# Optimization experiments

Measured on AMD Instinct MI355X. Metric: run time of the kernel, lower is better.

Reference implementation:

```python
import jax, jax.numpy as jnp
import numpy as np

D_MODEL = 1024
N_HEADS = 16
HEAD_DIM = 64
BATCH = 4
SEQ = 2048


def setup_inputs() -> dict:
    key = jax.random.key(0)
    ks = jax.random.split(key, 5)
    scale = 1.0 / np.sqrt(D_MODEL)
    return {
        "x": jax.random.normal(ks[0], (BATCH, SEQ, D_MODEL), dtype=jnp.float32),
        "Wq": jax.random.normal(ks[1], (D_MODEL, N_HEADS * HEAD_DIM), dtype=jnp.float32) * scale,
        "Wk": jax.random.normal(ks[2], (D_MODEL, N_HEADS * HEAD_DIM), dtype=jnp.float32) * scale,
        "Wv": jax.random.normal(ks[3], (D_MODEL, N_HEADS * HEAD_DIM), dtype=jnp.float32) * scale,
        "Wo": jax.random.normal(ks[4], (N_HEADS * HEAD_DIM, D_MODEL), dtype=jnp.float32) * scale,
        "bo": jnp.zeros((D_MODEL,), dtype=jnp.float32),
    }


def reference(x, Wq, Wk, Wv, Wo, bo):
    B, S, _ = x.shape
    H, Dh = N_HEADS, HEAD_DIM
    # projections -> [B, H, S, Dh]
    q = (x @ Wq).reshape(B, S, H, Dh).transpose(0, 2, 1, 3)
    k = (x @ Wk).reshape(B, S, H, Dh).transpose(0, 2, 1, 3)
    v = (x @ Wv).reshape(B, S, H, Dh).transpose(0, 2, 1, 3)
    score = jnp.einsum("bhsd,bhtd->bhst", q, k) / jnp.sqrt(jnp.float32(Dh))
    causal = jnp.triu(jnp.ones((S, S), dtype=bool), k=1)
    score = jnp.where(causal, -jnp.inf, score)
    attn_probs = jax.nn.softmax(score, axis=-1)
    # dropout is identity in eval mode
    attn = jnp.einsum("bhst,bhtd->bhsd", attn_probs, v)
    out = attn.transpose(0, 2, 1, 3).reshape(B, S, H * Dh)
    out = out @ Wo + bo
    return (out, attn_probs)
```

## Files before the change

kernel.cpp:

```cpp
#include <hip/hip_runtime.h>
#include <hip/hip_bf16.h>

typedef __attribute__((ext_vector_type(8))) short bf16x8;
typedef __attribute__((ext_vector_type(4))) float f32x4;
typedef unsigned short ushort_t;
typedef unsigned int uint_t;

#define AS1 __attribute__((address_space(1)))
#define AS3 __attribute__((address_space(3)))

__device__ __forceinline__ void gload_lds16(const void* g, void* l) {
    __builtin_amdgcn_global_load_lds((const AS1 void*)g, (AS3 void*)l, 16, 0, 0);
}

__device__ __forceinline__ ushort_t f2b(float f) {
    unsigned u = __builtin_bit_cast(unsigned, f);
    unsigned r = (u + 0x7FFFu + ((u >> 16) & 1u)) >> 16;
    return (ushort_t)r;
}

__global__ __launch_bounds__(256) void convert_x_kernel(const float* __restrict__ in,
                                                        ushort_t* __restrict__ out, int n4) {
    int i = blockIdx.x * blockDim.x + threadIdx.x;
    if (i < n4) {
        float4 f = ((const float4*)in)[i];
        ushort4 u;
        u.x = f2b(f.x); u.y = f2b(f.y); u.z = f2b(f.z); u.w = f2b(f.w);
        ((ushort4*)out)[i] = u;
    }
}

__global__ __launch_bounds__(256) void transpose_w_kernel(const float* __restrict__ W,
                                                          ushort_t* __restrict__ WT) {
    __shared__ float t[32][33];
    int n0 = blockIdx.x * 32, k0 = blockIdx.y * 32;
    int tx = threadIdx.x, ty = threadIdx.y;
    for (int i = 0; i < 4; ++i)
        t[ty + i * 8][tx] = W[(size_t)(k0 + ty + i * 8) * 1024 + n0 + tx];
    __syncthreads();
    for (int i = 0; i < 4; ++i)
        WT[(size_t)(n0 + ty + i * 8) * 1024 + k0 + tx] = f2b(t[tx][ty + i * 8]);
}

template <int N, int OUT_BF16>
__global__ __launch_bounds__(256) void gemm_kernel(const ushort_t* __restrict__ A,
                                                   const ushort_t* __restrict__ BT,
                                                   ushort_t* __restrict__ Cb,
                                                   float* __restrict__ Cf,
                                                   const float* __restrict__ bias) {
    const int K = 1024;
    __shared__ ushort_t As[2 * 128 * 32];
    __shared__ ushort_t Bs[2 * 128 * 32];
    int tid = threadIdx.x;
    int wid = tid >> 6, lane = tid & 63;
    int g = lane >> 4, lr = lane & 15;
    int m0 = blockIdx.x * 128, n0 = blockIdx.y * 128;
    int wm = wid >> 1, wn = wid & 1;

    f32x4 acc[4][4] = {};

    int c0 = wid * 2;
    int lrow = lane >> 2;
    int lcol = ((lane & 3) ^ ((lane >> 3) & 3)) * 8;
    const ushort_t* Ag0 = A  + (size_t)(m0 + c0 * 16 + lrow) * K + lcol;
    const ushort_t* Ag1 = A  + (size_t)(m0 + c0 * 16 + 16 + lrow) * K + lcol;
    const ushort_t* Bg0 = BT + (size_t)(n0 + c0 * 16 + lrow) * K + lcol;
    const ushort_t* Bg1 = BT + (size_t)(n0 + c0 * 16 + 16 + lrow) * K + lcol;

    int swzA = ((lr >> 1) & 3) << 4;

    auto stage = [&](int bufi, int kt) {
        char* a0 = (char*)As + bufi * 8192 + c0 * 1024;
        char* b0 = (char*)Bs + bufi * 8192 + c0 * 1024;
        gload_lds16(Ag0 + kt * 32, a0);
        gload_lds16(Ag1 + kt * 32, a0 + 1024);
        gload_lds16(Bg0 + kt * 32, b0);
        gload_lds16(Bg1 + kt * 32, b0 + 1024);
    };

    stage(0, 0);
    __syncthreads();
    int buf = 0;
    for (int kt = 0; kt < K / 32; ++kt) {
        if (kt + 1 < K / 32) stage(buf ^ 1, kt + 1);
        const char* ab = (const char*)As + buf * 8192;
        const char* bb = (const char*)Bs + buf * 8192;
        bf16x8 af[4], bfr[4];
#pragma unroll
        for (int m = 0; m < 4; ++m) {
            int row = wm * 64 + m * 16 + lr;
            af[m] = *(const bf16x8*)(ab + row * 64 + ((g * 16) ^ swzA));
        }
#pragma unroll
        for (int n = 0; n < 4; ++n) {
            int row = wn * 64 + n * 16 + lr;
            bfr[n] = *(const bf16x8*)(bb + row * 64 + ((g * 16) ^ swzA));
        }
#pragma unroll
        for (int m = 0; m < 4; ++m)
#pragma unroll
            for (int n = 0; n < 4; ++n)
                acc[m][n] = __builtin_amdgcn_mfma_f32_16x16x32_bf16(af[m], bfr[n], acc[m][n], 0, 0, 0);
        __syncthreads();
        buf ^= 1;
    }

#pragma unroll
    for (int m = 0; m < 4; ++m)
#pragma unroll
        for (int n = 0; n < 4; ++n) {
            int row0 = m0 + wm * 64 + m * 16 + g * 4;
            int col  = n0 + wn * 64 + n * 16 + lr;
#pragma unroll
            for (int r = 0; r < 4; ++r) {
                float v = acc[m][n][r];
                if (OUT_BF16)
                    Cb[(size_t)(row0 + r) * N + col] = f2b(v);
                else
                    Cf[(size_t)(row0 + r) * N + col] = v + bias[col];
            }
        }
}

__global__ __launch_bounds__(256) void vt_kernel(const ushort_t* __restrict__ Cqkv,
                                                 ushort_t* __restrict__ Vt) {
    int b = blockIdx.z, h = blockIdx.y, st = blockIdx.x;
    __shared__ ushort_t t[64][72];
    const ushort_t* src = Cqkv + (size_t)b * 2048 * 3072 + 2048 + (size_t)h * 64;
    int tid = threadIdx.x;
#pragma unroll
    for (int i = 0; i < 2; ++i) {
        int c = tid + i * 256;
        int sl = c >> 3, dc = (c & 7) * 8;
        *(bf16x8*)&t[sl][dc] = *(const bf16x8*)(src + (size_t)(st * 64 + sl) * 3072 + dc);
    }
    __syncthreads();
#pragma unroll
    for (int i = 0; i < 2; ++i) {
        int c = tid + i * 256;
        int d = c >> 3, sc = (c & 7) * 8;
        bf16x8 v;
#pragma unroll
        for (int j = 0; j < 8; ++j) v[j] = (short)t[sc + j][d];
        *(bf16x8*)(Vt + ((size_t)(b * 16 + h) * 64 + d) * 2048 + st * 64 + sc) = v;
    }
}

__global__ __launch_bounds__(256) void attn_kernel(const ushort_t* __restrict__ Cqkv,
                                                   const ushort_t* __restrict__ Vtg,
                                                   float* __restrict__ Pout,
                                                   ushort_t* __restrict__ Oout) {
    const int S = 2048, DQ = 3072;
    const float C1 = 0.18033688f;
    const float C2 = 5.77078016f;

    int z = (int)blockIdx.x + 32 * (int)blockIdx.y + 512 * (int)blockIdx.z;
    int h = (z >> 5) & 15, b = z >> 9;
    int qt = ((z & 31) + 13 * ((z >> 8) & 7)) & 31;
    int q0 = qt * 64;

    int tid = threadIdx.x, wid = tid >> 6, lane = tid & 63;
    int g = lane >> 4, lr = lane & 15;

    __shared__ ushort_t Ks[2][4096];
    __shared__ ushort_t Vs[2][4096];
    __shared__ ushort_t Pl[4096];
    char* PlB = (char*)Pl + wid * 2048;

    const ushort_t* Qb = Cqkv + (size_t)b * S * DQ + (size_t)h * 64;
    const ushort_t* Kb = Cqkv + (size_t)b * S * DQ + 1024 + (size_t)h * 64;
    const ushort_t* Vb = Vtg + (size_t)((b * 16 + h) * 64) * 2048;
    float* Pbase = Pout + (((size_t)(b * 16 + h)) * S + q0) * S;

    int srow = lane >> 3;
    int scol = ((lane & 7) ^ srow) * 8;

    auto stageK = [&](int bufi, int tt) {
        char* dst = (char*)&Ks[bufi][0] + wid * 1024;
        gload_lds16(Kb + (size_t)(tt * 64 + wid * 8 + srow) * DQ + scol, dst);
        gload_lds16(Kb + (size_t)(tt * 64 + 32 + wid * 8 + srow) * DQ + scol, dst + 4096);
    };
    auto stageV = [&](int bufi, int tt) {
        char* dst = (char*)&Vs[bufi][0] + wid * 1024;
        gload_lds16(Vb + (size_t)(wid * 8 + srow) * 2048 + tt * 64 + scol, dst);
        gload_lds16(Vb + (size_t)(32 + wid * 8 + srow) * 2048 + tt * 64 + scol, dst + 4096);
    };

    bf16x8 qf[2];
    {
        const ushort_t* qp = Qb + (size_t)(q0 + wid * 16 + lr) * DQ + g * 8;
        qf[0] = *(const bf16x8*)qp;
        qf[1] = *(const bf16x8*)(qp + 32);
    }
    int qloc = wid * 16 + lr;

    float psum = 0.f;
    stageK(0, 0);
    __syncthreads();
    int buf = 0;
    for (int tt = 0; tt <= qt; ++tt) {
        if (tt < qt) stageK(buf ^ 1, tt + 1);
        const char* ksb = (const char*)&Ks[buf][0];
#pragma unroll
        for (int nb = 0; nb < 4; ++nb) {
            int row = nb * 16 + lr;
            int x = (row & 7) << 4;
            f32x4 s = {};
            s = __builtin_amdgcn_mfma_f32_16x16x32_bf16(*(const bf16x8*)(ksb + row * 128 + ((g * 16) ^ x)), qf[0], s, 0, 0, 0);
            s = __builtin_amdgcn_mfma_f32_16x16x32_bf16(*(const bf16x8*)(ksb + row * 128 + ((64 + g * 16) ^ x)), qf[1], s, 0, 0, 0);
            if (tt == qt) {
#pragma unroll
                for (int r = 0; r < 4; ++r)
                    if (nb * 16 + g * 4 + r <= qloc) psum += exp2f(fmaf(s[r], C1, -C2));
            } else {
#pragma unroll
                for (int r = 0; r < 4; ++r) psum += exp2f(fmaf(s[r], C1, -C2));
            }
        }
        __syncthreads();
        buf ^= 1;
    }
    psum += __shfl_xor(psum, 16);
    psum += __shfl_xor(psum, 32);
    float lnl2 = __log2f(psum) + C2;

    f32x4 Oacc[4] = {};
    stageK(buf, 0);
    stageV(buf, 0);
    __syncthreads();
    for (int tt = 0; tt <= qt; ++tt) {
        if (tt < qt) { stageK(buf ^ 1, tt + 1); stageV(buf ^ 1, tt + 1); }
        const char* ksb = (const char*)&Ks[buf][0];
        const char* vsb = (const char*)&Vs[buf][0];
        f32x4 p[4];
#pragma unroll
        for (int nb = 0; nb < 4; ++nb) {
            int row = nb * 16 + lr;
            int x = (row & 7) << 4;
            f32x4 s = {};
            s = __builtin_amdgcn_mfma_f32_16x16x32_bf16(*(const bf16x8*)(ksb + row * 128 + ((g * 16) ^ x)), qf[0], s, 0, 0, 0);
            s = __builtin_amdgcn_mfma_f32_16x16x32_bf16(*(const bf16x8*)(ksb + row * 128 + ((64 + g * 16) ^ x)), qf[1], s, 0, 0, 0);
#pragma unroll
            for (int r = 0; r < 4; ++r) {
                float v = exp2f(fmaf(s[r], C1, -lnl2));
                if (tt == qt && (nb * 16 + g * 4 + r > qloc)) v = 0.f;
                p[nb][r] = v;
            }
        }
#pragma unroll
        for (int nb = 0; nb < 4; ++nb)
            *(f32x4*)(Pbase + (size_t)qloc * S + tt * 64 + nb * 16 + g * 4) = p[nb];
#pragma unroll
        for (int nb = 0; nb < 4; ++nb) {
            uint_t w0, w1;
            asm("v_cvt_pk_bf16_f32 %0, %1, %2" : "=v"(w0) : "v"(p[nb][0]), "v"(p[nb][1]));
            asm("v_cvt_pk_bf16_f32 %0, %1, %2" : "=v"(w1) : "v"(p[nb][2]), "v"(p[nb][3]));
            uint2 w; w.x = w0; w.y = w1;
            *(uint2*)(PlB + ((lr * 128 + nb * 32 + g * 8) ^ ((lr & 7) << 4))) = w;
        }
        __builtin_amdgcn_wave_barrier();
#pragma unroll
        for (int kc = 0; kc < 2; ++kc) {
            bf16x8 pf = *(const bf16x8*)(PlB + ((lr * 128 + kc * 64 + g * 16) ^ ((lr & 7) << 4)));
#pragma unroll
            for (int nb = 0; nb < 4; ++nb) {
                int vrow = nb * 16 + lr;
                bf16x8 vf = *(const bf16x8*)(vsb + vrow * 128 + ((kc * 64 + g * 16) ^ ((vrow & 7) << 4)));
                Oacc[nb] = __builtin_amdgcn_mfma_f32_16x16x32_bf16(pf, vf, Oacc[nb], 0, 0, 0);
            }
        }
        asm volatile("s_waitcnt vmcnt(4)" ::: "memory");
        __builtin_amdgcn_s_barrier();
        __builtin_amdgcn_sched_barrier(0);
        buf ^= 1;
    }

    {
        int vsr = tid >> 2, vsc = (tid & 3) * 16;
        float4 zf = {0.f, 0.f, 0.f, 0.f};
        for (int tt = qt + 1; tt < 32; ++tt) {
            float* dst = Pbase + (size_t)vsr * S + tt * 64 + vsc;
#pragma unroll
            for (int j = 0; j < 4; ++j) ((float4*)dst)[j] = zf;
        }
    }

#pragma unroll
    for (int nb = 0; nb < 4; ++nb)
#pragma unroll
        for (int r = 0; r < 4; ++r) {
            int q = q0 + wid * 16 + g * 4 + r;
            Oout[((size_t)b * S + q) * 1024 + h * 64 + nb * 16 + lr] = f2b(Oacc[nb][r]);
        }
}

extern "C" void kernel_launch(void* const* d_in, const int* in_sizes, int n_in,
                              void* d_out, int out_size, void* d_ws, size_t ws_size,
                              hipStream_t stream) {
    const float* x  = (const float*)d_in[0];
    const float* Wq = (const float*)d_in[1];
    const float* Wk = (const float*)d_in[2];
    const float* Wv = (const float*)d_in[3];
    const float* Wo = (const float*)d_in[4];
    const float* bo = (const float*)d_in[5];

    float* out  = (float*)d_out;
    float* Pout = out + (size_t)8388608;

    char* ws = (char*)d_ws;
    ushort_t* xb    = (ushort_t*)(ws);
    ushort_t* wqkv  = (ushort_t*)(ws + (16u << 20));
    ushort_t* wob   = (ushort_t*)(ws + (22u << 20));
    ushort_t* Cqkv  = (ushort_t*)(ws + (24u << 20));
    ushort_t* Vtw   = (ushort_t*)(ws + (72u << 20));
    ushort_t* attnb = (ushort_t*)(ws + (104u << 20));

    convert_x_kernel<<<8192, 256, 0, stream>>>(x, xb, 2097152);
    transpose_w_kernel<<<dim3(32, 32), dim3(32, 8), 0, stream>>>(Wq, wqkv);
    transpose_w_kernel<<<dim3(32, 32), dim3(32, 8), 0, stream>>>(Wk, wqkv + 1024 * 1024);
    transpose_w_kernel<<<dim3(32, 32), dim3(32, 8), 0, stream>>>(Wv, wqkv + 2 * 1024 * 1024);
    transpose_w_kernel<<<dim3(32, 32), dim3(32, 8), 0, stream>>>(Wo, wob);

    gemm_kernel<3072, 1><<<dim3(64, 24), 256, 0, stream>>>(xb, wqkv, Cqkv, nullptr, nullptr);

    vt_kernel<<<dim3(32, 16, 4), 256, 0, stream>>>(Cqkv, Vtw);

    attn_kernel<<<dim3(32, 16, 4), 256, 0, stream>>>(Cqkv, Vtw, Pout, attnb);

    gemm_kernel<1024, 0><<<dim3(64, 8), 256, 0, stream>>>(attnb, wob, nullptr, out, bo);
}
```

Before: 485.8 us.

## Fuse V transpose into QKV GEMM, remap GEMM blocks, deepen K prefetch, set wave priority

The QKV GEMM now writes the V columns straight into the transposed Vt layout, which removes the separate vt_kernel launch and its extra round trip through memory. Both GEMMs remap workgroup IDs in an XCD-aware order, aiming for better L2 locality. The first attention pass now keeps three K tiles in flight through a four-slot ring with vmcnt-based waits, and s_setprio is raised around the MFMA sections. The Vt stores from the GEMM are 8-byte strided writes, which may be less efficient than the old transpose kernel's writes.

```diff
diff --git a/kernel.cpp b/kernel.cpp
--- a/kernel.cpp
+++ b/kernel.cpp
@@ -42,19 +42,25 @@
         WT[(size_t)(n0 + ty + i * 8) * 1024 + k0 + tx] = f2b(t[tx][ty + i * 8]);
 }
 
-template <int N, int OUT_BF16>
+template <int N, int MODE>
 __global__ __launch_bounds__(256) void gemm_kernel(const ushort_t* __restrict__ A,
                                                    const ushort_t* __restrict__ BT,
                                                    ushort_t* __restrict__ Cb,
                                                    float* __restrict__ Cf,
-                                                   const float* __restrict__ bias) {
+                                                   const float* __restrict__ bias,
+                                                   ushort_t* __restrict__ Vt) {
     const int K = 1024;
     __shared__ ushort_t As[2 * 128 * 32];
     __shared__ ushort_t Bs[2 * 128 * 32];
     int tid = threadIdx.x;
     int wid = tid >> 6, lane = tid & 63;
     int g = lane >> 4, lr = lane & 15;
-    int m0 = blockIdx.x * 128, n0 = blockIdx.y * 128;
+
+    int z = (int)blockIdx.x + 64 * (int)blockIdx.y;
+    int nwg = 64 * (int)gridDim.y;
+    int zs = (z & 7) * (nwg >> 3) + (z >> 3);
+    int m0 = (zs % 64) * 128, n0 = (zs / 64) * 128;
+
     int wm = wid >> 1, wn = wid & 1;
 
     f32x4 acc[4][4] = {};
@@ -105,44 +111,35 @@
         buf ^= 1;
     }
 
-#pragma unroll
-    for (int m = 0; m < 4; ++m)
-#pragma unroll
-        for (int n = 0; n < 4; ++n) {
-            int row0 = m0 + wm * 64 + m * 16 + g * 4;
-            int col  = n0 + wn * 64 + n * 16 + lr;
-#pragma unroll
-            for (int r = 0; r < 4; ++r) {
-                float v = acc[m][n][r];
-                if (OUT_BF16)
-                    Cb[(size_t)(row0 + r) * N + col] = f2b(v);
-                else
-                    Cf[(size_t)(row0 + r) * N + col] = v + bias[col];
-            }
-        }
-}
-
-__global__ __launch_bounds__(256) void vt_kernel(const ushort_t* __restrict__ Cqkv,
-                                                 ushort_t* __restrict__ Vt) {
-    int b = blockIdx.z, h = blockIdx.y, st = blockIdx.x;
-    __shared__ ushort_t t[64][72];
-    const ushort_t* src = Cqkv + (size_t)b * 2048 * 3072 + 2048 + (size_t)h * 64;
-    int tid = threadIdx.x;
-#pragma unroll
-    for (int i = 0; i < 2; ++i) {
-        int c = tid + i * 256;
-        int sl = c >> 3, dc = (c & 7) * 8;
-        *(bf16x8*)&t[sl][dc] = *(const bf16x8*)(src + (size_t)(st * 64 + sl) * 3072 + dc);
-    }
-    __syncthreads();
-#pragma unroll
-    for (int i = 0; i < 2; ++i) {
-        int c = tid + i * 256;
-        int d = c >> 3, sc = (c & 7) * 8;
-        bf16x8 v;
-#pragma unroll
-        for (int j = 0; j < 8; ++j) v[j] = (short)t[sc + j][d];
-        *(bf16x8*)(Vt + ((size_t)(b * 16 + h) * 64 + d) * 2048 + st * 64 + sc) = v;
+    if (MODE == 2 && (n0 + wn * 64) >= 2048) {
+#pragma unroll
+        for (int m = 0; m < 4; ++m)
+#pragma unroll
+            for (int n = 0; n < 4; ++n) {
+                int row0 = m0 + wm * 64 + m * 16 + g * 4;
+                int c    = n0 + wn * 64 + n * 16 + lr - 2048;
+                int bb2 = row0 >> 11, sloc = row0 & 2047;
+                ushort4 u;
+                u.x = f2b(acc[m][n][0]); u.y = f2b(acc[m][n][1]);
+                u.z = f2b(acc[m][n][2]); u.w = f2b(acc[m][n][3]);
+                *(ushort4*)(Vt + ((size_t)(bb2 * 1024 + c)) * 2048 + sloc) = u;
+            }
+    } else {
+#pragma unroll
+        for (int m = 0; m < 4; ++m)
+#pragma unroll
+            for (int n = 0; n < 4; ++n) {
+                int row0 = m0 + wm * 64 + m * 16 + g * 4;
+                int col  = n0 + wn * 64 + n * 16 + lr;
+#pragma unroll
+                for (int r = 0; r < 4; ++r) {
+                    float v = acc[m][n][r];
+                    if (MODE == 0)
+                        Cf[(size_t)(row0 + r) * N + col] = v + bias[col];
+                    else
+                        Cb[(size_t)(row0 + r) * N + col] = f2b(v);
+                }
+            }
     }
 }
 
@@ -162,8 +159,7 @@
     int tid = threadIdx.x, wid = tid >> 6, lane = tid & 63;
     int g = lane >> 4, lr = lane & 15;
 
-    __shared__ ushort_t Ks[2][4096];
-    __shared__ ushort_t Vs[2][4096];
+    __shared__ ushort_t KV[4][4096];
     __shared__ ushort_t Pl[4096];
     char* PlB = (char*)Pl + wid * 2048;
 
@@ -175,13 +171,13 @@
     int srow = lane >> 3;
     int scol = ((lane & 7) ^ srow) * 8;
 
-    auto stageK = [&](int bufi, int tt) {
-        char* dst = (char*)&Ks[bufi][0] + wid * 1024;
+    auto stageK = [&](int ri, int tt) {
+        char* dst = (char*)&KV[ri][0] + wid * 1024;
         gload_lds16(Kb + (size_t)(tt * 64 + wid * 8 + srow) * DQ + scol, dst);
         gload_lds16(Kb + (size_t)(tt * 64 + 32 + wid * 8 + srow) * DQ + scol, dst + 4096);
     };
-    auto stageV = [&](int bufi, int tt) {
-        char* dst = (char*)&Vs[bufi][0] + wid * 1024;
+    auto stageV = [&](int ri, int tt) {
+        char* dst = (char*)&KV[2 + ri][0] + wid * 1024;
         gload_lds16(Vb + (size_t)(wid * 8 + srow) * 2048 + tt * 64 + scol, dst);
         gload_lds16(Vb + (size_t)(32 + wid * 8 + srow) * 2048 + tt * 64 + scol, dst + 4096);
     };
@@ -196,11 +192,15 @@
 
     float psum = 0.f;
     stageK(0, 0);
-    __syncthreads();
-    int buf = 0;
+    stageK(1, qt >= 1 ? 1 : 0);
+    asm volatile("s_waitcnt vmcnt(8)" ::: "memory");
+    __builtin_amdgcn_s_barrier();
+    __builtin_amdgcn_sched_barrier(0);
     for (int tt = 0; tt <= qt; ++tt) {
-        if (tt < qt) stageK(buf ^ 1, tt + 1);
-        const char* ksb = (const char*)&Ks[buf][0];
+        int nt = tt + 2;
+        stageK(nt & 3, nt <= qt ? nt : qt);
+        const char* ksb = (const char*)&KV[tt & 3][0];
+        __builtin_amdgcn_s_setprio(1);
 #pragma unroll
         for (int nb = 0; nb < 4; ++nb) {
             int row = nb * 16 + lr;
@@ -217,22 +217,26 @@
                 for (int r = 0; r < 4; ++r) psum += exp2f(fmaf(s[r], C1, -C2));
             }
         }
-        __syncthreads();
-        buf ^= 1;
+        __builtin_amdgcn_s_setprio(0);
+        asm volatile("s_waitcnt vmcnt(8)" ::: "memory");
+        __builtin_amdgcn_s_barrier();
+        __builtin_amdgcn_sched_barrier(0);
     }
     psum += __shfl_xor(psum, 16);
     psum += __shfl_xor(psum, 32);
     float lnl2 = __log2f(psum) + C2;
 
     f32x4 Oacc[4] = {};
-    stageK(buf, 0);
-    stageV(buf, 0);
+    stageK(0, 0);
+    stageV(0, 0);
     __syncthreads();
+    int buf = 0;
     for (int tt = 0; tt <= qt; ++tt) {
         if (tt < qt) { stageK(buf ^ 1, tt + 1); stageV(buf ^ 1, tt + 1); }
-        const char* ksb = (const char*)&Ks[buf][0];
-        const char* vsb = (const char*)&Vs[buf][0];
+        const char* ksb = (const char*)&KV[buf][0];
+        const char* vsb = (const char*)&KV[2 + buf][0];
         f32x4 p[4];
+        __builtin_amdgcn_s_setprio(1);
 #pragma unroll
         for (int nb = 0; nb < 4; ++nb) {
             int row = nb * 16 + lr;
@@ -247,6 +251,7 @@
                 p[nb][r] = v;
             }
         }
+        __builtin_amdgcn_s_setprio(0);
 #pragma unroll
         for (int nb = 0; nb < 4; ++nb)
             *(f32x4*)(Pbase + (size_t)qloc * S + tt * 64 + nb * 16 + g * 4) = p[nb];
@@ -259,6 +264,7 @@
             *(uint2*)(PlB + ((lr * 128 + nb * 32 + g * 8) ^ ((lr & 7) << 4))) = w;
         }
         __builtin_amdgcn_wave_barrier();
+        __builtin_amdgcn_s_setprio(1);
 #pragma unroll
         for (int kc = 0; kc < 2; ++kc) {
             bf16x8 pf = *(const bf16x8*)(PlB + ((lr * 128 + kc * 64 + g * 16) ^ ((lr & 7) << 4)));
@@ -269,6 +275,7 @@
                 Oacc[nb] = __builtin_amdgcn_mfma_f32_16x16x32_bf16(pf, vf, Oacc[nb], 0, 0, 0);
             }
         }
+        __builtin_amdgcn_s_setprio(0);
         asm volatile("s_waitcnt vmcnt(4)" ::: "memory");
         __builtin_amdgcn_s_barrier();
         __builtin_amdgcn_sched_barrier(0);
@@ -321,11 +328,9 @@
     transpose_w_kernel<<<dim3(32, 32), dim3(32, 8), 0, stream>>>(Wv, wqkv + 2 * 1024 * 1024);
     transpose_w_kernel<<<dim3(32, 32), dim3(32, 8), 0, stream>>>(Wo, wob);
 
-    gemm_kernel<3072, 1><<<dim3(64, 24), 256, 0, stream>>>(xb, wqkv, Cqkv, nullptr, nullptr);
-
-    vt_kernel<<<dim3(32, 16, 4), 256, 0, stream>>>(Cqkv, Vtw);
+    gemm_kernel<3072, 2><<<dim3(64, 24), 256, 0, stream>>>(xb, wqkv, Cqkv, nullptr, nullptr, Vtw);
 
     attn_kernel<<<dim3(32, 16, 4), 256, 0, stream>>>(Cqkv, Vtw, Pout, attnb);
 
-    gemm_kernel<1024, 0><<<dim3(64, 8), 256, 0, stream>>>(attnb, wob, nullptr, out, bo);
-}
+    gemm_kernel<1024, 0><<<dim3(64, 8), 256, 0, stream>>>(attnb, wob, nullptr, out, bo, nullptr);
+}
```

Measured after the change: 508.8 us. +4.7%, slower.

## Restructure attention for occupancy, triple-buffer GEMM, remap GEMM blocks, merge weight transposes

Applied to the files above, without the earlier changes.

Several changes at once. The attention kernel shrinks LDS to single-buffered K/V with a smaller P scratch and adds launch bounds for higher occupancy. It also interleaves the zero-fill of masked probability tiles into the main loops and uses s_setprio around MFMA sections. The GEMM moves to a three-stage LDS pipeline with explicit vmcnt waits and a remapped block order for cache locality. The four weight transposes merge into one launch. The cost is that attention loses its K/V prefetch overlap in the second pass.

```diff
diff --git a/kernel.cpp b/kernel.cpp
--- a/kernel.cpp
+++ b/kernel.cpp
@@ -30,9 +30,16 @@
     }
 }
 
-__global__ __launch_bounds__(256) void transpose_w_kernel(const float* __restrict__ W,
-                                                          ushort_t* __restrict__ WT) {
+__global__ __launch_bounds__(256) void transpose_w4_kernel(const float* __restrict__ W0,
+                                                           const float* __restrict__ W1,
+                                                           const float* __restrict__ W2,
+                                                           const float* __restrict__ W3,
+                                                           ushort_t* __restrict__ WTqkv,
+                                                           ushort_t* __restrict__ WTo) {
     __shared__ float t[32][33];
+    int which = blockIdx.z;
+    const float* W = (which == 0) ? W0 : (which == 1) ? W1 : (which == 2) ? W2 : W3;
+    ushort_t* WT = (which < 3) ? (WTqkv + (size_t)which * 1024 * 1024) : WTo;
     int n0 = blockIdx.x * 32, k0 = blockIdx.y * 32;
     int tx = threadIdx.x, ty = threadIdx.y;
     for (int i = 0; i < 4; ++i)
@@ -49,12 +56,17 @@
                                                    float* __restrict__ Cf,
                                                    const float* __restrict__ bias) {
     const int K = 1024;
-    __shared__ ushort_t As[2 * 128 * 32];
-    __shared__ ushort_t Bs[2 * 128 * 32];
+    __shared__ ushort_t As[3 * 128 * 32];
+    __shared__ ushort_t Bs[3 * 128 * 32];
     int tid = threadIdx.x;
     int wid = tid >> 6, lane = tid & 63;
     int g = lane >> 4, lr = lane & 15;
-    int m0 = blockIdx.x * 128, n0 = blockIdx.y * 128;
+
+    int zz = (int)blockIdx.x + 64 * (int)blockIdx.y;
+    int nwg = 64 * (int)gridDim.y;
+    int zs = (zz & 7) * (nwg >> 3) + (zz >> 3);
+    int m0 = (zs % 64) * 128, n0 = (zs / 64) * 128;
+
     int wm = wid >> 1, wn = wid & 1;
 
     f32x4 acc[4][4] = {};
@@ -69,9 +81,9 @@
 
     int swzA = ((lr >> 1) & 3) << 4;
 
-    auto stage = [&](int bufi, int kt) {
-        char* a0 = (char*)As + bufi * 8192 + c0 * 1024;
-        char* b0 = (char*)Bs + bufi * 8192 + c0 * 1024;
+    auto stage = [&](int si, int kt) {
+        char* a0 = (char*)As + si * 8192 + c0 * 1024;
+        char* b0 = (char*)Bs + si * 8192 + c0 * 1024;
         gload_lds16(Ag0 + kt * 32, a0);
         gload_lds16(Ag1 + kt * 32, a0 + 1024);
         gload_lds16(Bg0 + kt * 32, b0);
@@ -79,12 +91,15 @@
     };
 
     stage(0, 0);
-    __syncthreads();
-    int buf = 0;
-    for (int kt = 0; kt < K / 32; ++kt) {
-        if (kt + 1 < K / 32) stage(buf ^ 1, kt + 1);
-        const char* ab = (const char*)As + buf * 8192;
-        const char* bb = (const char*)Bs + buf * 8192;
+    stage(1, 1);
+    asm volatile("s_waitcnt vmcnt(4)" ::: "memory");
+    __builtin_amdgcn_s_barrier();
+    __builtin_amdgcn_sched_barrier(0);
+    for (int kt = 0; kt < 32; ++kt) {
+        int nt = kt + 2;
+        stage(nt % 3, nt < 32 ? nt : 31);
+        const char* ab = (const char*)As + (kt % 3) * 8192;
+        const char* bb = (const char*)Bs + (kt % 3) * 8192;
         bf16x8 af[4], bfr[4];
 #pragma unroll
         for (int m = 0; m < 4; ++m) {
@@ -101,8 +116,9 @@
 #pragma unroll
             for (int n = 0; n < 4; ++n)
                 acc[m][n] = __builtin_amdgcn_mfma_f32_16x16x32_bf16(af[m], bfr[n], acc[m][n], 0, 0, 0);
-        __syncthreads();
-        buf ^= 1;
+        asm volatile("s_waitcnt vmcnt(4)" ::: "memory");
+        __builtin_amdgcn_s_barrier();
+        __builtin_amdgcn_sched_barrier(0);
     }
 
 #pragma unroll
@@ -146,10 +162,10 @@
     }
 }
 
-__global__ __launch_bounds__(256) void attn_kernel(const ushort_t* __restrict__ Cqkv,
-                                                   const ushort_t* __restrict__ Vtg,
-                                                   float* __restrict__ Pout,
-                                                   ushort_t* __restrict__ Oout) {
+__global__ __launch_bounds__(256, 6) void attn_kernel(const ushort_t* __restrict__ Cqkv,
+                                                      const ushort_t* __restrict__ Vtg,
+                                                      float* __restrict__ Pout,
+                                                      ushort_t* __restrict__ Oout) {
     const int S = 2048, DQ = 3072;
     const float C1 = 0.18033688f;
     const float C2 = 5.77078016f;
@@ -161,11 +177,12 @@
 
     int tid = threadIdx.x, wid = tid >> 6, lane = tid & 63;
     int g = lane >> 4, lr = lane & 15;
-
-    __shared__ ushort_t Ks[2][4096];
-    __shared__ ushort_t Vs[2][4096];
-    __shared__ ushort_t Pl[4096];
-    char* PlB = (char*)Pl + wid * 2048;
+    int vsr = tid >> 2, vsc = (tid & 3) * 16;
+
+    __shared__ ushort_t Ks[4096];
+    __shared__ ushort_t Vs[4096];
+    __shared__ ushort_t Pl[2048];
+    char* PlB = (char*)Pl + wid * 1024;
 
     const ushort_t* Qb = Cqkv + (size_t)b * S * DQ + (size_t)h * 64;
     const ushort_t* Kb = Cqkv + (size_t)b * S * DQ + 1024 + (size_t)h * 64;
@@ -175,13 +192,21 @@
     int srow = lane >> 3;
     int scol = ((lane & 7) ^ srow) * 8;
 
-    auto stageK = [&](int bufi, int tt) {
-        char* dst = (char*)&Ks[bufi][0] + wid * 1024;
+    int zcount = 31 - qt, zi = 0;
+    auto zfill = [&](int k) {
+        float* dst = Pbase + (size_t)vsr * S + (qt + 1 + k) * 64 + vsc;
+        f32x4 zf = {0.f, 0.f, 0.f, 0.f};
+#pragma unroll
+        for (int jj = 0; jj < 4; ++jj) ((f32x4*)dst)[jj] = zf;
+    };
+
+    auto stageKto = [&](char* base, int tt) {
+        char* dst = base + wid * 1024;
         gload_lds16(Kb + (size_t)(tt * 64 + wid * 8 + srow) * DQ + scol, dst);
         gload_lds16(Kb + (size_t)(tt * 64 + 32 + wid * 8 + srow) * DQ + scol, dst + 4096);
     };
-    auto stageV = [&](int bufi, int tt) {
-        char* dst = (char*)&Vs[bufi][0] + wid * 1024;
+    auto stageVto = [&](int tt) {
+        char* dst = (char*)Vs + wid * 1024;
         gload_lds16(Vb + (size_t)(wid * 8 + srow) * 2048 + tt * 64 + scol, dst);
         gload_lds16(Vb + (size_t)(32 + wid * 8 + srow) * 2048 + tt * 64 + scol, dst + 4096);
     };
@@ -194,16 +219,19 @@
     }
     int qloc = wid * 16 + lr;
 
-    float psum = 0.f;
-    stageK(0, 0);
-    __syncthreads();
-    int buf = 0;
+    float ps = 0.f;
+    stageKto((char*)Ks, 0);
+    asm volatile("s_waitcnt vmcnt(0)" ::: "memory");
+    __builtin_amdgcn_s_barrier();
+    __builtin_amdgcn_sched_barrier(0);
     for (int tt = 0; tt <= qt; ++tt) {
-        if (tt < qt) stageK(buf ^ 1, tt + 1);
-        const char* ksb = (const char*)&Ks[buf][0];
-#pragma unroll
-        for (int nb = 0; nb < 4; ++nb) {
-            int row = nb * 16 + lr;
+        if (zi < zcount) zfill(zi++);
+        if (tt < qt) stageKto((tt & 1) ? (char*)Ks : (char*)Vs, tt + 1);
+        const char* ksb = (tt & 1) ? (const char*)Vs : (const char*)Ks;
+        __builtin_amdgcn_s_setprio(1);
+#pragma unroll
+        for (int tb = 0; tb < 4; ++tb) {
+            int row = tb * 16 + lr;
             int x = (row & 7) << 4;
             f32x4 s = {};
             s = __builtin_amdgcn_mfma_f32_16x16x32_bf16(*(const bf16x8*)(ksb + row * 128 + ((g * 16) ^ x)), qf[0], s, 0, 0, 0);
@@ -211,86 +239,85 @@
             if (tt == qt) {
 #pragma unroll
                 for (int r = 0; r < 4; ++r)
-                    if (nb * 16 + g * 4 + r <= qloc) psum += exp2f(fmaf(s[r], C1, -C2));
+                    if (tb * 16 + g * 4 + r <= qloc) ps += exp2f(fmaf(s[r], C1, -C2));
             } else {
 #pragma unroll
-                for (int r = 0; r < 4; ++r) psum += exp2f(fmaf(s[r], C1, -C2));
+                for (int r = 0; r < 4; ++r) ps += exp2f(fmaf(s[r], C1, -C2));
             }
         }
-        __syncthreads();
-        buf ^= 1;
-    }
-    psum += __shfl_xor(psum, 16);
-    psum += __shfl_xor(psum, 32);
-    float lnl2 = __log2f(psum) + C2;
-
-    f32x4 Oacc[4] = {};
-    stageK(buf, 0);
-    stageV(buf, 0);
-    __syncthreads();
-    for (int tt = 0; tt <= qt; ++tt) {
-        if (tt < qt) { stageK(buf ^ 1, tt + 1); stageV(buf ^ 1, tt + 1); }
-        const char* ksb = (const char*)&Ks[buf][0];
-        const char* vsb = (const char*)&Vs[buf][0];
-        f32x4 p[4];
-#pragma unroll
-        for (int nb = 0; nb < 4; ++nb) {
-            int row = nb * 16 + lr;
-            int x = (row & 7) << 4;
-            f32x4 s = {};
-            s = __builtin_amdgcn_mfma_f32_16x16x32_bf16(*(const bf16x8*)(ksb + row * 128 + ((g * 16) ^ x)), qf[0], s, 0, 0, 0);
-            s = __builtin_amdgcn_mfma_f32_16x16x32_bf16(*(const bf16x8*)(ksb + row * 128 + ((64 + g * 16) ^ x)), qf[1], s, 0, 0, 0);
-#pragma unroll
-            for (int r = 0; r < 4; ++r) {
-                float v = exp2f(fmaf(s[r], C1, -lnl2));
-                if (tt == qt && (nb * 16 + g * 4 + r > qloc)) v = 0.f;
-                p[nb][r] = v;
-            }
-        }
-#pragma unroll
-        for (int nb = 0; nb < 4; ++nb)
-            *(f32x4*)(Pbase + (size_t)qloc * S + tt * 64 + nb * 16 + g * 4) = p[nb];
-#pragma unroll
-        for (int nb = 0; nb < 4; ++nb) {
-            uint_t w0, w1;
-            asm("v_cvt_pk_bf16_f32 %0, %1, %2" : "=v"(w0) : "v"(p[nb][0]), "v"(p[nb][1]));
-            asm("v_cvt_pk_bf16_f32 %0, %1, %2" : "=v"(w1) : "v"(p[nb][2]), "v"(p[nb][3]));
-            uint2 w; w.x = w0; w.y = w1;
-            *(uint2*)(PlB + ((lr * 128 + nb * 32 + g * 8) ^ ((lr & 7) << 4))) = w;
-        }
-        __builtin_amdgcn_wave_barrier();
-#pragma unroll
-        for (int kc = 0; kc < 2; ++kc) {
-            bf16x8 pf = *(const bf16x8*)(PlB + ((lr * 128 + kc * 64 + g * 16) ^ ((lr & 7) << 4)));
-#pragma unroll
-            for (int nb = 0; nb < 4; ++nb) {
-                int vrow = nb * 16 + lr;
-                bf16x8 vf = *(const bf16x8*)(vsb + vrow * 128 + ((kc * 64 + g * 16) ^ ((vrow & 7) << 4)));
-                Oacc[nb] = __builtin_amdgcn_mfma_f32_16x16x32_bf16(pf, vf, Oacc[nb], 0, 0, 0);
-            }
-        }
-        asm volatile("s_waitcnt vmcnt(4)" ::: "memory");
+        __builtin_amdgcn_s_setprio(0);
+        asm volatile("s_waitcnt vmcnt(0)" ::: "memory");
         __builtin_amdgcn_s_barrier();
         __builtin_amdgcn_sched_barrier(0);
-        buf ^= 1;
-    }
-
-    {
-        int vsr = tid >> 2, vsc = (tid & 3) * 16;
-        float4 zf = {0.f, 0.f, 0.f, 0.f};
-        for (int tt = qt + 1; tt < 32; ++tt) {
-            float* dst = Pbase + (size_t)vsr * S + tt * 64 + vsc;
-#pragma unroll
-            for (int j = 0; j < 4; ++j) ((float4*)dst)[j] = zf;
-        }
-    }
-
-#pragma unroll
-    for (int nb = 0; nb < 4; ++nb)
+    }
+    ps += __shfl_xor(ps, 16);
+    ps += __shfl_xor(ps, 32);
+    float lnl = __log2f(ps) + C2;
+
+    f32x4 OA[4] = {};
+    stageKto((char*)Ks, 0);
+    stageVto(0);
+    asm volatile("s_waitcnt vmcnt(0)" ::: "memory");
+    __builtin_amdgcn_s_barrier();
+    __builtin_amdgcn_sched_barrier(0);
+    for (int tt = 0; tt <= qt; ++tt) {
+        if (zi < zcount) zfill(zi++);
+        if (zi < zcount) zfill(zi++);
+        const char* ksb = (const char*)Ks;
+        const char* vsb = (const char*)Vs;
+#pragma unroll
+        for (int half = 0; half < 2; ++half) {
+            __builtin_amdgcn_s_setprio(1);
+#pragma unroll
+            for (int tbl = 0; tbl < 2; ++tbl) {
+                int tb = half * 2 + tbl;
+                int row = tb * 16 + lr;
+                int x = (row & 7) << 4;
+                f32x4 s = {};
+                s = __builtin_amdgcn_mfma_f32_16x16x32_bf16(*(const bf16x8*)(ksb + row * 128 + ((g * 16) ^ x)), qf[0], s, 0, 0, 0);
+                s = __builtin_amdgcn_mfma_f32_16x16x32_bf16(*(const bf16x8*)(ksb + row * 128 + ((64 + g * 16) ^ x)), qf[1], s, 0, 0, 0);
+                f32x4 pv;
+#pragma unroll
+                for (int r = 0; r < 4; ++r) {
+                    float v = exp2f(fmaf(s[r], C1, -lnl));
+                    if (tt == qt && (tb * 16 + g * 4 + r > qloc)) v = 0.f;
+                    pv[r] = v;
+                }
+                *(f32x4*)(Pbase + (size_t)qloc * S + tt * 64 + tb * 16 + g * 4) = pv;
+                uint_t w0, w1;
+                asm("v_cvt_pk_bf16_f32 %0, %1, %2" : "=v"(w0) : "v"(pv[0]), "v"(pv[1]));
+                asm("v_cvt_pk_bf16_f32 %0, %1, %2" : "=v"(w1) : "v"(pv[2]), "v"(pv[3]));
+                uint2 w; w.x = w0; w.y = w1;
+                *(uint2*)(PlB + lr * 64 + tbl * 32 + g * 8) = w;
+            }
+            __builtin_amdgcn_s_setprio(0);
+            __builtin_amdgcn_wave_barrier();
+            bf16x8 pf = *(const bf16x8*)(PlB + lr * 64 + g * 16);
+            __builtin_amdgcn_s_setprio(1);
+#pragma unroll
+            for (int db = 0; db < 4; ++db) {
+                int vrow = db * 16 + lr;
+                bf16x8 vf = *(const bf16x8*)(vsb + vrow * 128 + ((half * 64 + g * 16) ^ ((vrow & 7) << 4)));
+                OA[db] = __builtin_amdgcn_mfma_f32_16x16x32_bf16(pf, vf, OA[db], 0, 0, 0);
+            }
+            __builtin_amdgcn_s_setprio(0);
+            __builtin_amdgcn_wave_barrier();
+        }
+        __builtin_amdgcn_s_barrier();
+        if (tt < qt) { stageKto((char*)Ks, tt + 1); stageVto(tt + 1); }
+        asm volatile("s_waitcnt vmcnt(0)" ::: "memory");
+        __builtin_amdgcn_s_barrier();
+        __builtin_amdgcn_sched_barrier(0);
+    }
+
+    while (zi < zcount) zfill(zi++);
+
+#pragma unroll
+    for (int db = 0; db < 4; ++db)
 #pragma unroll
         for (int r = 0; r < 4; ++r) {
             int q = q0 + wid * 16 + g * 4 + r;
-            Oout[((size_t)b * S + q) * 1024 + h * 64 + nb * 16 + lr] = f2b(Oacc[nb][r]);
+            Oout[((size_t)b * S + q) * 1024 + h * 64 + db * 16 + lr] = f2b(OA[db][r]);
         }
 }
 
@@ -316,10 +343,7 @@
     ushort_t* attnb = (ushort_t*)(ws + (104u << 20));
 
     convert_x_kernel<<<8192, 256, 0, stream>>>(x, xb, 2097152);
-    transpose_w_kernel<<<dim3(32, 32), dim3(32, 8), 0, stream>>>(Wq, wqkv);
-    transpose_w_kernel<<<dim3(32, 32), dim3(32, 8), 0, stream>>>(Wk, wqkv + 1024 * 1024);
-    transpose_w_kernel<<<dim3(32, 32), dim3(32, 8), 0, stream>>>(Wv, wqkv + 2 * 1024 * 1024);
-    transpose_w_kernel<<<dim3(32, 32), dim3(32, 8), 0, stream>>>(Wo, wob);
+    transpose_w4_kernel<<<dim3(32, 32, 4), dim3(32, 8), 0, stream>>>(Wq, Wk, Wv, Wo, wqkv, wob);
 
     gemm_kernel<3072, 1><<<dim3(64, 24), 256, 0, stream>>>(xb, wqkv, Cqkv, nullptr, nullptr);
 
```

Result: slower. 516.1 us (+6.2%).
